# Performance work log

Measured on AMD Instinct MI355X. Metric: run time of the kernel, lower is better.

Reference implementation:

```python
import jax, jax.numpy as jnp
import numpy as np

D = 512        # feat_dim
H_ENC = 8      # motion_encoder heads
H_SA = 4       # semantic-aware attention heads
BS, L, N = 8, 512, 4096
LN_EPS = 1e-5


def _layernorm(x, g, b):
    m = jnp.mean(x, axis=-1, keepdims=True)
    v = jnp.var(x, axis=-1, keepdims=True)
    return (x - m) * jax.lax.rsqrt(v + LN_EPS) * g + b


def _linear(x, w, b):
    # torch nn.Linear convention: w [out, in]
    return x @ w.T + b


def setup_inputs() -> dict:
    key = jax.random.key(0)
    ks = jax.random.split(key, 24)
    s = 0.02
    inp = {
        "motion": jax.random.normal(ks[0], (BS, L, D), jnp.float32),
        "scene_xyz": jax.random.normal(ks[1], (BS, N, 3), jnp.float32),
        "scene_feats": jax.random.normal(ks[2], (BS, N, D), jnp.float32),
        "spatial_prior": jax.random.normal(ks[3], (BS, L, N), jnp.float32),
        # motion_encoder (pre-norm MHA + pre-norm MLP, both residual)
        "enc_ln1_g": jnp.ones((D,), jnp.float32),
        "enc_ln1_b": jnp.zeros((D,), jnp.float32),
        "enc_qkv_w": jax.random.normal(ks[4], (3 * D, D), jnp.float32) * s,
        "enc_qkv_b": jnp.zeros((3 * D,), jnp.float32),
        "enc_out_w": jax.random.normal(ks[5], (D, D), jnp.float32) * s,
        "enc_out_b": jnp.zeros((D,), jnp.float32),
        "enc_ln2_g": jnp.ones((D,), jnp.float32),
        "enc_ln2_b": jnp.zeros((D,), jnp.float32),
        "enc_ff1_w": jax.random.normal(ks[6], (D, D), jnp.float32) * s,
        "enc_ff1_b": jnp.zeros((D,), jnp.float32),
        "enc_ff2_w": jax.random.normal(ks[7], (D, D), jnp.float32) * s,
        "enc_ff2_b": jnp.zeros((D,), jnp.float32),
        # SemanticAwareAttention
        "sa_q_w": jax.random.normal(ks[8], (D, D), jnp.float32) * s,
        "sa_q_b": jnp.zeros((D,), jnp.float32),
        "sa_kv_w": jax.random.normal(ks[9], (2 * D, D), jnp.float32) * s,
        "sa_kv_b": jnp.zeros((2 * D,), jnp.float32),
        "sa_out_w": jax.random.normal(ks[10], (D, D), jnp.float32) * s,
        "sa_out_b": jnp.zeros((D,), jnp.float32),
        # final concat-MLP: in 2D -> 4D -> D  (Mlp(2D, D, expansion=4))
        "mlp_fc1_w": jax.random.normal(ks[11], (4 * D, 2 * D), jnp.float32) * s,
        "mlp_fc1_b": jnp.zeros((4 * D,), jnp.float32),
        "mlp_fc2_w": jax.random.normal(ks[12], (D, 4 * D), jnp.float32) * s,
        "mlp_fc2_b": jnp.zeros((D,), jnp.float32),
    }
    return inp


def _forward(motion, scene_xyz, scene_feats, spatial_prior,
             enc_ln1_g, enc_ln1_b, enc_qkv_w, enc_qkv_b, enc_out_w, enc_out_b,
             enc_ln2_g, enc_ln2_b, enc_ff1_w, enc_ff1_b, enc_ff2_w, enc_ff2_b,
             sa_q_w, sa_q_b, sa_kv_w, sa_kv_b, sa_out_w, sa_out_b,
             mlp_fc1_w, mlp_fc1_b, mlp_fc2_w, mlp_fc2_b):
    bs, slen, _ = motion.shape
    n = scene_feats.shape[1]
    dh_enc = D // H_ENC
    dh_sa = D // H_SA

    # ---- motion encoder: pre-norm MHA + residual ----
    h = _layernorm(motion, enc_ln1_g, enc_ln1_b)
    qkv = _linear(h, enc_qkv_w, enc_qkv_b)                      # [bs, L, 3D]
    q, k, v = jnp.split(qkv, 3, axis=-1)
    q = q.reshape(bs, slen, H_ENC, dh_enc)
    k = k.reshape(bs, slen, H_ENC, dh_enc)
    v = v.reshape(bs, slen, H_ENC, dh_enc)
    att = jnp.einsum("bqhd,bkhd->bhqk", q, k) * (dh_enc ** -0.5)
    att = jax.nn.softmax(att, axis=-1)
    o = jnp.einsum("bhqk,bkhd->bqhd", att, v).reshape(bs, slen, D)
    x = motion + _linear(o, enc_out_w, enc_out_b)

    # ---- pre-norm MLP + residual ----
    h2 = _layernorm(x, enc_ln2_g, enc_ln2_b)
    ff = _linear(jax.nn.gelu(_linear(h2, enc_ff1_w, enc_ff1_b), approximate=False),
                 enc_ff2_w, enc_ff2_b)
    motion_sca = x + ff

    # ---- SemanticAwareAttention ----
    q = _linear(motion_sca, sa_q_w, sa_q_b) * (D ** -0.5)       # scale by feat_dim (faithful)
    kv = _linear(scene_feats, sa_kv_w, sa_kv_b)
    k, v = jnp.split(kv, 2, axis=-1)
    # faithful to torch: q.view(bs, H, L, d) splits heads from flattened (L, D)
    q = q.reshape(bs, H_SA, slen, dh_sa)
    k = k.reshape(bs, n, H_SA, dh_sa).transpose(0, 2, 1, 3)     # [bs, H, N, d]
    v = v.reshape(bs, n, H_SA, dh_sa).transpose(0, 2, 1, 3)
    att = jnp.einsum("bhqd,bhkd->bhqk", q, k) + spatial_prior[:, None, :, :]
    att = jax.nn.softmax(att, axis=-1)
    sm = jnp.einsum("bhqk,bhkd->bqhd", att, v).reshape(bs, slen, D)
    sm_feature = _linear(sm, sa_out_w, sa_out_b)

    # ---- concat + MLP ----
    cat = jnp.concatenate([motion_sca, sm_feature], axis=-1)    # [bs, L, 2D]
    out = _linear(jax.nn.gelu(_linear(cat, mlp_fc1_w, mlp_fc1_b), approximate=False),
                  mlp_fc2_w, mlp_fc2_b)
    return out


def reference(motion, scene_xyz, scene_feats, spatial_prior,
              enc_ln1_g, enc_ln1_b, enc_qkv_w, enc_qkv_b, enc_out_w, enc_out_b,
              enc_ln2_g, enc_ln2_b, enc_ff1_w, enc_ff1_b, enc_ff2_w, enc_ff2_b,
              sa_q_w, sa_q_b, sa_kv_w, sa_kv_b, sa_out_w, sa_out_b,
              mlp_fc1_w, mlp_fc1_b, mlp_fc2_w, mlp_fc2_b):
    return _forward(motion, scene_xyz, scene_feats, spatial_prior,
                    enc_ln1_g, enc_ln1_b, enc_qkv_w, enc_qkv_b, enc_out_w, enc_out_b,
                    enc_ln2_g, enc_ln2_b, enc_ff1_w, enc_ff1_b, enc_ff2_w, enc_ff2_b,
                    sa_q_w, sa_q_b, sa_kv_w, sa_kv_b, sa_out_w, sa_out_b,
                    mlp_fc1_w, mlp_fc1_b, mlp_fc2_w, mlp_fc2_b)
```

## Files before the change

kernel.cpp:

```cpp
#include <hip/hip_runtime.h>

typedef unsigned short bf16_t;
typedef __attribute__((ext_vector_type(8))) short bf16x8;
typedef __attribute__((ext_vector_type(4))) float f32x4;

__device__ __forceinline__ float bf2f(bf16_t u) {
  union { unsigned int i; float f; } v; v.i = ((unsigned int)u) << 16; return v.f;
}
__device__ __forceinline__ bf16_t f2bf(float f) {
  union { float f; unsigned int i; } v; v.f = f;
  unsigned int u = v.i;
  u += 0x7fffu + ((u >> 16) & 1u);
  return (bf16_t)(u >> 16);
}
__device__ __forceinline__ float gelu_exact(float x) {
  return 0.5f * x * (1.0f + erff(x * 0.7071067811865475f));
}
__device__ __forceinline__ void g2l16(bf16_t* l, const bf16_t* g) {
  __builtin_amdgcn_global_load_lds(
      (const __attribute__((address_space(1))) unsigned int*)g,
      (__attribute__((address_space(3))) unsigned int*)l, 16, 0, 0);
}

__global__ __launch_bounds__(256) void f2bf_kernel(const float4* __restrict__ s,
                                                   ushort4* __restrict__ d, int n4) {
  int i = blockIdx.x * 256 + threadIdx.x;
  if (i < n4) {
    float4 f = s[i];
    ushort4 u; u.x = f2bf(f.x); u.y = f2bf(f.y); u.z = f2bf(f.z); u.w = f2bf(f.w);
    d[i] = u;
  }
}

__global__ __launch_bounds__(256) void ln_kernel(const float* __restrict__ x,
                                                 const float* __restrict__ g,
                                                 const float* __restrict__ bta,
                                                 bf16_t* __restrict__ y) {
  const int w = threadIdx.x >> 6, lane = threadIdx.x & 63;
  const long row = (long)blockIdx.x * 4 + w;
  const long base = row * 512;
  const int c0 = lane << 2;
  float v[8];
  float4 f0 = *(const float4*)(x + base + c0);
  float4 f1 = *(const float4*)(x + base + 256 + c0);
  v[0]=f0.x; v[1]=f0.y; v[2]=f0.z; v[3]=f0.w;
  v[4]=f1.x; v[5]=f1.y; v[6]=f1.z; v[7]=f1.w;
  float s = 0.f;
#pragma unroll
  for (int c=0;c<8;++c) s += v[c];
#pragma unroll
  for (int o=32;o>0;o>>=1) s += __shfl_xor(s, o);
  const float mean = s * 0.001953125f;
  float ss = 0.f;
#pragma unroll
  for (int c=0;c<8;++c) { float d = v[c]-mean; ss += d*d; }
#pragma unroll
  for (int o=32;o>0;o>>=1) ss += __shfl_xor(ss, o);
  const float rstd = rsqrtf(ss * 0.001953125f + 1e-5f);
  ushort4 o0, o1;
  o0.x = f2bf((v[0]-mean)*rstd*g[c0+0] + bta[c0+0]);
  o0.y = f2bf((v[1]-mean)*rstd*g[c0+1] + bta[c0+1]);
  o0.z = f2bf((v[2]-mean)*rstd*g[c0+2] + bta[c0+2]);
  o0.w = f2bf((v[3]-mean)*rstd*g[c0+3] + bta[c0+3]);
  o1.x = f2bf((v[4]-mean)*rstd*g[256+c0+0] + bta[256+c0+0]);
  o1.y = f2bf((v[5]-mean)*rstd*g[256+c0+1] + bta[256+c0+1]);
  o1.z = f2bf((v[6]-mean)*rstd*g[256+c0+2] + bta[256+c0+2]);
  o1.w = f2bf((v[7]-mean)*rstd*g[256+c0+3] + bta[256+c0+3]);
  *(ushort4*)(y + base + c0) = o0;
  *(ushort4*)(y + base + 256 + c0) = o1;
}

struct MmaNT {
  const bf16_t* A; const bf16_t* W; const float* bias; const float* res; void* C;
  long lda, sAb, sAh;
  long ldw, sWb, sWh;
  long ldr, sRb, sRh;
  long ldc, sCb, sCh;
  int K, zdiv, cBf, act;
  float scale;
};

template <int MT>
__global__ __launch_bounds__(256) void mma_nt_kernel(MmaNT p) {
  constexpr int FM = MT / 32;
  constexpr int TILE_E = (MT + 128) * 32;
  constexpr int ST_E = MT * 128;
  constexpr int SM_E = (TILE_E > ST_E) ? TILE_E : ST_E;
  __shared__ __align__(16) bf16_t smem[SM_E];
  bf16_t* Al = smem;
  bf16_t* Wl = smem + MT * 32;
  const int tid = threadIdx.x;
  const int wid = tid >> 6, lane = tid & 63;
  const int wm = wid & 1, wn = wid >> 1;
  const int quad = lane >> 4, l16 = lane & 15;
  const int z = blockIdx.z;
  const int zb = z / p.zdiv, zh = z % p.zdiv;

  const int nbx = gridDim.x;
  const int nwg = nbx * gridDim.y;
  const int flat = blockIdx.y * nbx + blockIdx.x;
  const int sw = (flat & 7) * (nwg >> 3) + (flat >> 3);
  const int bx = sw % nbx, by = sw / nbx;

  const long m0 = (long)by * MT;
  const long n0 = (long)bx * 128;

  f32x4 zero4 = {0.f, 0.f, 0.f, 0.f};
  f32x4 acc[FM][4];
#pragma unroll
  for (int fm = 0; fm < FM; ++fm)
#pragma unroll
    for (int fn = 0; fn < 4; ++fn) acc[fm][fn] = zero4;

  if constexpr (MT == 128) {
    const bf16_t* Ag = p.A + (long)zb * p.sAb + (long)zh * p.sAh + m0 * p.lda;
    const bf16_t* Wg = p.W + (long)zb * p.sWb + (long)zh * p.sWh + n0 * p.ldw;
    const int sr = lane >> 2;
    const int sc = (lane & 3) * 8;
    for (int kc = 0; kc < p.K; kc += 32) {
#pragma unroll
      for (int j = 0; j < 2; ++j)
        g2l16(&Al[(j * 64 + wid * 16) * 32],
              Ag + (long)(j * 64 + wid * 16 + sr) * p.lda + kc + sc);
#pragma unroll
      for (int j = 0; j < 2; ++j)
        g2l16(&Wl[(j * 64 + wid * 16) * 32],
              Wg + (long)(j * 64 + wid * 16 + sr) * p.ldw + kc + sc);
      __syncthreads();
      bf16x8 af[FM], wf[4];
#pragma unroll
      for (int fm = 0; fm < FM; ++fm)
        af[fm] = *(const bf16x8*)&Al[(wm * 64 + fm * 16 + l16) * 32 + quad * 8];
#pragma unroll
      for (int fn = 0; fn < 4; ++fn)
        wf[fn] = *(const bf16x8*)&Wl[(wn * 64 + fn * 16 + l16) * 32 + quad * 8];
#pragma unroll
      for (int fm = 0; fm < FM; ++fm)
#pragma unroll
        for (int fn = 0; fn < 4; ++fn)
          acc[fm][fn] = __builtin_amdgcn_mfma_f32_16x16x32_bf16(af[fm], wf[fn], acc[fm][fn], 0, 0, 0);
      __syncthreads();
    }
  } else {
    const bf16_t* Ag = p.A + (long)zb * p.sAb + (long)zh * p.sAh +
                       (m0 + wm * (MT / 2) + l16) * p.lda;
    const bf16_t* Wg = p.W + (long)zb * p.sWb + (long)zh * p.sWh +
                       (n0 + wn * 64 + l16) * p.ldw;
    bf16x8 af[FM], wf[4];
#pragma unroll
    for (int fm = 0; fm < FM; ++fm)
      af[fm] = *(const bf16x8*)(Ag + (long)(fm * 16) * p.lda + quad * 8);
#pragma unroll
    for (int fn = 0; fn < 4; ++fn)
      wf[fn] = *(const bf16x8*)(Wg + (long)(fn * 16) * p.ldw + quad * 8);
    for (int kc = 0; kc < p.K; kc += 32) {
      bf16x8 afn[FM], wfn[4];
      const int kn = kc + 32;
      if (kn < p.K) {
#pragma unroll
        for (int fm = 0; fm < FM; ++fm)
          afn[fm] = *(const bf16x8*)(Ag + (long)(fm * 16) * p.lda + kn + quad * 8);
#pragma unroll
        for (int fn = 0; fn < 4; ++fn)
          wfn[fn] = *(const bf16x8*)(Wg + (long)(fn * 16) * p.ldw + kn + quad * 8);
      }
#pragma unroll
      for (int fm = 0; fm < FM; ++fm)
#pragma unroll
        for (int fn = 0; fn < 4; ++fn)
          acc[fm][fn] = __builtin_amdgcn_mfma_f32_16x16x32_bf16(af[fm], wf[fn], acc[fm][fn], 0, 0, 0);
#pragma unroll
      for (int fm = 0; fm < FM; ++fm) af[fm] = afn[fm];
#pragma unroll
      for (int fn = 0; fn < 4; ++fn) wf[fn] = wfn[fn];
    }
  }

  const long cOff = (long)zb * p.sCb + (long)zh * p.sCh;
  const long rOff = (long)zb * p.sRb + (long)zh * p.sRh;
  if (p.cBf) {
#pragma unroll
    for (int fm = 0; fm < FM; ++fm) {
#pragma unroll
      for (int fn = 0; fn < 4; ++fn) {
        const int lc = wn * 64 + fn * 16 + l16;
        const long col = n0 + lc;
        const float bv = p.bias ? p.bias[col] : 0.f;
#pragma unroll
        for (int r = 0; r < 4; ++r) {
          const int lr = wm * (MT / 2) + fm * 16 + quad * 4 + r;
          float t = acc[fm][fn][r] + bv;
          if (p.act) t = gelu_exact(t);
          t *= p.scale;
          if (p.res) t += p.res[rOff + (m0 + lr) * p.ldr + col];
          smem[lr * 128 + lc] = f2bf(t);
        }
      }
    }
    __syncthreads();
    bf16_t* Cg = (bf16_t*)p.C + cOff + m0 * p.ldc + n0;
#pragma unroll
    for (int i = 0; i < MT / 16; ++i) {
      const int flat2 = tid + i * 256;
      const int r = flat2 >> 4, c = (flat2 & 15) * 8;
      *(uint4*)(Cg + (long)r * p.ldc + c) = *(const uint4*)&smem[r * 128 + c];
    }
  } else {
#pragma unroll
    for (int fm = 0; fm < FM; ++fm) {
#pragma unroll
      for (int fn = 0; fn < 4; ++fn) {
        const long col = n0 + wn * 64 + fn * 16 + l16;
        const float bv = p.bias ? p.bias[col] : 0.f;
#pragma unroll
        for (int r = 0; r < 4; ++r) {
          const long row = m0 + wm * (MT / 2) + fm * 16 + quad * 4 + r;
          float t = acc[fm][fn][r] + bv;
          if (p.act) t = gelu_exact(t);
          t *= p.scale;
          if (p.res) t += p.res[rOff + row * p.ldr + col];
          ((float*)p.C)[cOff + row * p.ldc + col] = t;
        }
      }
    }
  }
}

struct TransP {
  const bf16_t* src; bf16_t* dst;
  long sSb, sSh, ld;
  int nh, N, D;
};

__global__ __launch_bounds__(256) void transpose_kernel(TransP p) {
  __shared__ bf16_t T[64][72];
  const int tid = threadIdx.x;
  const int z = blockIdx.z;
  const int zb = z / p.nh, zh = z % p.nh;
  const long n0 = (long)blockIdx.x * 64;
  const long d0 = (long)blockIdx.y * 64;
  const bf16_t* src = p.src + (long)zb * p.sSb + (long)zh * p.sSh;
  bf16_t* dst = p.dst + (long)z * p.D * p.N;
#pragma unroll
  for (int i = 0; i < 2; ++i) {
    int flat = tid + i * 256, r = flat >> 3, cg = flat & 7;
    uint4 v = *(const uint4*)(src + (n0 + r) * p.ld + d0 + cg * 8);
    *(uint4*)&T[r][cg * 8] = v;
  }
  __syncthreads();
#pragma unroll
  for (int i = 0; i < 2; ++i) {
    int flat = tid + i * 256, dr = flat >> 3, ncg = flat & 7;
    uint4 o;
    unsigned int* op = (unsigned int*)&o;
#pragma unroll
    for (int j = 0; j < 4; ++j)
      op[j] = (unsigned int)T[ncg * 8 + 2 * j][dr] | ((unsigned int)T[ncg * 8 + 2 * j + 1][dr] << 16);
    *(uint4*)(dst + (d0 + dr) * p.N + n0 + ncg * 8) = o;
  }
}

struct FlashP2 {
  const bf16_t* Q; const bf16_t* K; const bf16_t* VT; const float* prior;
  float* partO; float* partML;
  long ldq, sQb, sQh;
  long ldk, sKb, sKh;
  long sVz, sPb;
  int nh, N, segN;
  float scale;
};

template <int DH, int HASP>
__global__ __launch_bounds__(256) void flash3_kernel(FlashP2 p) {
  constexpr int KK = DH / 32;
  constexpr int NFO = DH / 16;
  constexpr int KPAD = DH + 8;
  __shared__ bf16_t smem[64 * KPAD + DH * 72];
  bf16_t* Kl = smem;
  bf16_t* Pl = smem;
  bf16_t* Vl = smem + 64 * KPAD;
  const int tid = threadIdx.x;
  const int w = tid >> 6, lane = tid & 63;
  const int quad = lane >> 4, l16 = lane & 15;
  const int z = blockIdx.z;
  const int zb = z / p.nh, zh = z % p.nh;
  const int qr0 = blockIdx.y * 64 + w * 16;
  const bf16_t* Q = p.Q + (long)zb * p.sQb + (long)zh * p.sQh + (long)qr0 * p.ldq;
  const bf16_t* K = p.K + (long)zb * p.sKb + (long)zh * p.sKh;
  const bf16_t* VT = p.VT + (long)z * p.sVz;

  bf16x8 qf[KK];
#pragma unroll
  for (int kk = 0; kk < KK; ++kk)
    qf[kk] = *(const bf16x8*)(Q + (long)l16 * p.ldq + kk * 32 + quad * 8);

  f32x4 zero4 = {0.f, 0.f, 0.f, 0.f};
  f32x4 O[NFO];
  float m_[4], l_[4];
#pragma unroll
  for (int f = 0; f < NFO; ++f) O[f] = zero4;
#pragma unroll
  for (int r = 0; r < 4; ++r) { m_[r] = -1e30f; l_[r] = 0.f; }

  const int k0 = blockIdx.x * p.segN;
  for (int kt = k0; kt < k0 + p.segN; kt += 64) {
    __syncthreads();
    constexpr int KTH = DH / 8;
#pragma unroll
    for (int i = 0; i < DH / 32; ++i) {
      int flat = tid + i * 256, r = flat / KTH, c = (flat % KTH) * 8;
      *(uint4*)&Kl[r * KPAD + c] = *(const uint4*)(K + (long)(kt + r) * p.ldk + c);
    }
#pragma unroll
    for (int i = 0; i < DH / 32; ++i) {
      int flat = tid + i * 256, r = flat >> 3, c = (flat & 7) * 8;
      *(uint4*)&Vl[r * 72 + c] = *(const uint4*)(VT + (long)r * p.N + kt + c);
    }
    float pr[4][4];
    if (HASP) {
      const float* PR = p.prior + (long)zb * p.sPb +
                        (long)(qr0 + quad * 4) * p.N + kt;
#pragma unroll
      for (int nf = 0; nf < 4; ++nf)
#pragma unroll
        for (int r = 0; r < 4; ++r)
          pr[nf][r] = PR[(long)r * p.N + nf * 16 + l16];
    }
    __syncthreads();
    f32x4 s[4];
#pragma unroll
    for (int nf = 0; nf < 4; ++nf) s[nf] = zero4;
#pragma unroll
    for (int nf = 0; nf < 4; ++nf)
#pragma unroll
      for (int kk = 0; kk < KK; ++kk) {
        bf16x8 kf = *(const bf16x8*)&Kl[(nf * 16 + l16) * KPAD + kk * 32 + quad * 8];
        s[nf] = __builtin_amdgcn_mfma_f32_16x16x32_bf16(qf[kk], kf, s[nf], 0, 0, 0);
      }
    float tm[4];
#pragma unroll
    for (int r = 0; r < 4; ++r) tm[r] = -1e30f;
#pragma unroll
    for (int nf = 0; nf < 4; ++nf)
#pragma unroll
      for (int r = 0; r < 4; ++r) {
        float t = s[nf][r] * p.scale;
        if (HASP) t += pr[nf][r];
        s[nf][r] = t;
        tm[r] = fmaxf(tm[r], t);
      }
#pragma unroll
    for (int off = 1; off < 16; off <<= 1)
#pragma unroll
      for (int r = 0; r < 4; ++r) tm[r] = fmaxf(tm[r], __shfl_xor(tm[r], off));
    float alpha[4], rs[4];
#pragma unroll
    for (int r = 0; r < 4; ++r) {
      float mn = fmaxf(m_[r], tm[r]);
      alpha[r] = __expf(m_[r] - mn);
      m_[r] = mn;
      rs[r] = 0.f;
    }
#pragma unroll
    for (int nf = 0; nf < 4; ++nf)
#pragma unroll
      for (int r = 0; r < 4; ++r) {
        float pv = __expf(s[nf][r] - m_[r]);
        s[nf][r] = pv;
        rs[r] += pv;
      }
#pragma unroll
    for (int off = 1; off < 16; off <<= 1)
#pragma unroll
      for (int r = 0; r < 4; ++r) rs[r] += __shfl_xor(rs[r], off);
#pragma unroll
    for (int r = 0; r < 4; ++r) l_[r] = l_[r] * alpha[r] + rs[r];
    __syncthreads();
#pragma unroll
    for (int nf = 0; nf < 4; ++nf)
#pragma unroll
      for (int r = 0; r < 4; ++r)
        Pl[(w * 16 + quad * 4 + r) * 72 + nf * 16 + l16] = f2bf(s[nf][r]);
#pragma unroll
    for (int f = 0; f < NFO; ++f)
#pragma unroll
      for (int r = 0; r < 4; ++r) O[f][r] *= alpha[r];
    bf16x8 pf[2];
#pragma unroll
    for (int kk2 = 0; kk2 < 2; ++kk2)
      pf[kk2] = *(const bf16x8*)&Pl[(w * 16 + l16) * 72 + kk2 * 32 + quad * 8];
#pragma unroll
    for (int f = 0; f < NFO; ++f)
#pragma unroll
      for (int kk2 = 0; kk2 < 2; ++kk2) {
        bf16x8 vf = *(const bf16x8*)&Vl[(f * 16 + l16) * 72 + kk2 * 32 + quad * 8];
        O[f] = __builtin_amdgcn_mfma_f32_16x16x32_bf16(pf[kk2], vf, O[f], 0, 0, 0);
      }
  }
  const long t = ((long)z * gridDim.y + blockIdx.y) * gridDim.x + blockIdx.x;
  float* PO = p.partO + t * (64 * DH);
  float* PM = p.partML + t * 128;
  const int row = w * 16 + quad * 4;
#pragma unroll
  for (int f = 0; f < NFO; ++f)
#pragma unroll
    for (int r = 0; r < 4; ++r)
      PO[(long)(row + r) * DH + f * 16 + l16] = O[f][r];
  if (l16 == 0) {
#pragma unroll
    for (int r = 0; r < 4; ++r) {
      PM[(row + r) * 2 + 0] = m_[r];
      PM[(row + r) * 2 + 1] = l_[r];
    }
  }
}

struct MergeP {
  const float* partO; const float* partML; bf16_t* C;
  long ldc, sCb;
  int nh, y;
};

template <int DH, int NS>
__global__ __launch_bounds__(256) void fmerge_kernel(MergeP p) {
  const int tid = threadIdx.x;
  const int r = tid >> 2, ch = tid & 3;
  const int blk = blockIdx.x;
  const int z = blk / p.y, qb = blk % p.y;
  const int zb = z / p.nh, zh = z % p.nh;
  const long t0 = (long)blk * NS;
  float mm[NS], wgt[NS];
  float mstar = -1e30f;
#pragma unroll
  for (int s = 0; s < NS; ++s) {
    mm[s] = p.partML[(t0 + s) * 128 + r * 2];
    mstar = fmaxf(mstar, mm[s]);
  }
  float lsum = 0.f;
#pragma unroll
  for (int s = 0; s < NS; ++s) {
    wgt[s] = __expf(mm[s] - mstar);
    lsum += wgt[s] * p.partML[(t0 + s) * 128 + r * 2 + 1];
  }
  const float inv = 1.0f / lsum;
  const int c0 = ch * (DH / 4);
  bf16_t* Cp = p.C + (long)zb * p.sCb + (long)(qb * 64 + r) * p.ldc + (long)zh * DH + c0;
#pragma unroll
  for (int c = 0; c < DH / 4; c += 4) {
    float4 acc = make_float4(0.f, 0.f, 0.f, 0.f);
#pragma unroll
    for (int s = 0; s < NS; ++s) {
      float4 v = *(const float4*)(p.partO + (t0 + s) * (64 * DH) + (long)r * DH + c0 + c);
      acc.x += wgt[s] * v.x; acc.y += wgt[s] * v.y;
      acc.z += wgt[s] * v.z; acc.w += wgt[s] * v.w;
    }
    ushort4 o;
    o.x = f2bf(acc.x * inv); o.y = f2bf(acc.y * inv);
    o.z = f2bf(acc.z * inv); o.w = f2bf(acc.w * inv);
    *(ushort4*)(Cp + c) = o;
  }
}

#define MB(x) ((long)(x) << 20)

extern "C" void kernel_launch(void* const* d_in, const int* in_sizes, int n_in,
                              void* d_out, int out_size, void* d_ws, size_t ws_size,
                              hipStream_t stream) {
  const float* motion      = (const float*)d_in[0];
  const float* scene_feats = (const float*)d_in[2];
  const float* prior       = (const float*)d_in[3];
  const float* ln1_g = (const float*)d_in[4];
  const float* ln1_b = (const float*)d_in[5];
  const float* qkv_w = (const float*)d_in[6];
  const float* qkv_b = (const float*)d_in[7];
  const float* out_w = (const float*)d_in[8];
  const float* out_b = (const float*)d_in[9];
  const float* ln2_g = (const float*)d_in[10];
  const float* ln2_b = (const float*)d_in[11];
  const float* ff1_w = (const float*)d_in[12];
  const float* ff1_b = (const float*)d_in[13];
  const float* ff2_w = (const float*)d_in[14];
  const float* ff2_b = (const float*)d_in[15];
  const float* saq_w = (const float*)d_in[16];
  const float* saq_b = (const float*)d_in[17];
  const float* sakv_w = (const float*)d_in[18];
  const float* sakv_b = (const float*)d_in[19];
  const float* saout_w = (const float*)d_in[20];
  const float* saout_b = (const float*)d_in[21];
  const float* fc1_w = (const float*)d_in[22];
  const float* fc1_b = (const float*)d_in[23];
  const float* fc2_w = (const float*)d_in[24];
  const float* fc2_b = (const float*)d_in[25];

  char* W = (char*)d_ws;
  bf16_t* h_bf    = (bf16_t*)(W + MB(0));
  float*  x_f     = (float*) (W + MB(4));
  bf16_t* o_ff    = (bf16_t*)(W + MB(12));
  bf16_t* qkv_bf  = (bf16_t*)(W + MB(16));
  bf16_t* qsa     = (bf16_t*)(W + MB(28));
  bf16_t* sm_bf   = (bf16_t*)(W + MB(32));
  bf16_t* cat_bf  = (bf16_t*)(W + MB(36));
  bf16_t* fc1g    = (bf16_t*)(W + MB(44));
  bf16_t* vTe     = (bf16_t*)(W + MB(60));
  bf16_t* kv_bf   = (bf16_t*)(W + MB(64));
  bf16_t* vT      = (bf16_t*)(W + MB(128));
  bf16_t* wbase   = (bf16_t*)(W + MB(160));
  bf16_t* scene_bf= (bf16_t*)(W + MB(172));

  float* encO  = (float*)fc1g;
  float* encML = (float*)cat_bf;
  float* saO   = (float*)scene_bf;
  float* saML  = (float*)vTe;

  bf16_t* wq   = wbase + 0L;
  bf16_t* wout = wbase + 786432L;
  bf16_t* wff1 = wbase + 1048576L;
  bf16_t* wff2 = wbase + 1310720L;
  bf16_t* wsaq = wbase + 1572864L;
  bf16_t* wskv = wbase + 1835008L;
  bf16_t* wsout= wbase + 2359296L;
  bf16_t* wfc1 = wbase + 2621440L;
  bf16_t* wfc2 = wbase + 4718592L;

  const dim3 B256(256);
  auto cvt = [&](const float* s, bf16_t* d, long n) {
    int n4 = (int)(n / 4);
    f2bf_kernel<<<(n4 + 255) / 256, B256, 0, stream>>>((const float4*)s, (ushort4*)d, n4);
  };
  cvt(qkv_w,  wq,   786432);
  cvt(out_w,  wout, 262144);
  cvt(ff1_w,  wff1, 262144);
  cvt(ff2_w,  wff2, 262144);
  cvt(saq_w,  wsaq, 262144);
  cvt(sakv_w, wskv, 524288);
  cvt(saout_w,wsout,262144);
  cvt(fc1_w,  wfc1, 2097152);
  cvt(fc2_w,  wfc2, 1048576);
  cvt(scene_feats, scene_bf, 16777216);

  ln_kernel<<<1024, B256, 0, stream>>>(motion, ln1_g, ln1_b, h_bf);

  { MmaNT p{}; p.scale=1.f; p.zdiv=1; p.cBf=1;
    p.A=h_bf; p.lda=512; p.W=wq; p.ldw=512; p.bias=qkv_b;
    p.C=qkv_bf; p.ldc=1536; p.K=512;
    mma_nt_kernel<128><<<dim3(12,32,1), B256, 0, stream>>>(p); }

  { TransP t{}; t.src=qkv_bf+1024; t.dst=vTe; t.sSb=786432; t.sSh=64;
    t.ld=1536; t.nh=8; t.N=512; t.D=64;
    transpose_kernel<<<dim3(8,1,64), B256, 0, stream>>>(t); }
  { FlashP2 p{};
    p.Q=qkv_bf;     p.ldq=1536; p.sQb=786432; p.sQh=64;
    p.K=qkv_bf+512; p.ldk=1536; p.sKb=786432; p.sKh=64;
    p.VT=vTe; p.sVz=32768;
    p.prior=nullptr; p.sPb=0;
    p.partO=encO; p.partML=encML;
    p.nh=8; p.N=512; p.segN=256; p.scale=0.125f;
    flash3_kernel<64,0><<<dim3(2,8,64), B256, 0, stream>>>(p); }
  { MergeP m{}; m.partO=encO; m.partML=encML; m.C=o_ff;
    m.ldc=512; m.sCb=262144; m.nh=8; m.y=8;
    fmerge_kernel<64,2><<<512, B256, 0, stream>>>(m); }

  { MmaNT p{}; p.scale=1.f; p.zdiv=1;
    p.A=o_ff; p.lda=512; p.W=wout; p.ldw=512; p.bias=out_b;
    p.res=motion; p.ldr=512;
    p.C=x_f; p.ldc=512; p.K=512;
    mma_nt_kernel<64><<<dim3(4,64,1), B256, 0, stream>>>(p); }

  ln_kernel<<<1024, B256, 0, stream>>>(x_f, ln2_g, ln2_b, h_bf);

  { MmaNT p{}; p.scale=1.f; p.zdiv=1; p.cBf=1; p.act=1;
    p.A=h_bf; p.lda=512; p.W=wff1; p.ldw=512; p.bias=ff1_b;
    p.C=o_ff; p.ldc=512; p.K=512;
    mma_nt_kernel<64><<<dim3(4,64,1), B256, 0, stream>>>(p); }

  { MmaNT p{}; p.scale=1.f; p.zdiv=1; p.cBf=1;
    p.A=o_ff; p.lda=512; p.W=wff2; p.ldw=512; p.bias=ff2_b;
    p.res=x_f; p.ldr=512;
    p.C=cat_bf; p.ldc=1024; p.K=512;
    mma_nt_kernel<64><<<dim3(4,64,1), B256, 0, stream>>>(p); }

  { MmaNT p{}; p.zdiv=1; p.cBf=1; p.scale=0.04419417382415922f;
    p.A=cat_bf; p.lda=1024; p.W=wsaq; p.ldw=512; p.bias=saq_b;
    p.C=qsa; p.ldc=512; p.K=512;
    mma_nt_kernel<64><<<dim3(4,64,1), B256, 0, stream>>>(p); }

  { MmaNT p{}; p.scale=1.f; p.zdiv=1; p.cBf=1;
    p.A=scene_bf; p.lda=512; p.W=wskv; p.ldw=512; p.bias=sakv_b;
    p.C=kv_bf; p.ldc=1024; p.K=512;
    mma_nt_kernel<128><<<dim3(8,256,1), B256, 0, stream>>>(p); }

  { TransP t{}; t.src=kv_bf+512; t.dst=vT; t.sSb=4194304; t.sSh=128;
    t.ld=1024; t.nh=4; t.N=4096; t.D=128;
    transpose_kernel<<<dim3(64,2,32), B256, 0, stream>>>(t); }
  { FlashP2 p{};
    p.Q=qsa;   p.ldq=128;  p.sQb=262144;  p.sQh=65536;
    p.K=kv_bf; p.ldk=1024; p.sKb=4194304; p.sKh=128;
    p.VT=vT; p.sVz=524288;
    p.prior=prior; p.sPb=2097152;
    p.partO=saO; p.partML=saML;
    p.nh=4; p.N=4096; p.segN=1024; p.scale=1.f;
    flash3_kernel<128,1><<<dim3(4,8,32), B256, 0, stream>>>(p); }
  { MergeP m{}; m.partO=saO; m.partML=saML; m.C=sm_bf;
    m.ldc=512; m.sCb=262144; m.nh=4; m.y=8;
    fmerge_kernel<128,4><<<256, B256, 0, stream>>>(m); }

  { MmaNT p{}; p.scale=1.f; p.zdiv=1; p.cBf=1;
    p.A=sm_bf; p.lda=512; p.W=wsout; p.ldw=512; p.bias=saout_b;
    p.C=cat_bf + 512; p.ldc=1024; p.K=512;
    mma_nt_kernel<64><<<dim3(4,64,1), B256, 0, stream>>>(p); }

  { MmaNT p{}; p.scale=1.f; p.zdiv=1; p.cBf=1; p.act=1;
    p.A=cat_bf; p.lda=1024; p.W=wfc1; p.ldw=1024; p.bias=fc1_b;
    p.C=fc1g; p.ldc=2048; p.K=1024;
    mma_nt_kernel<128><<<dim3(16,32,1), B256, 0, stream>>>(p); }

  { MmaNT p{}; p.scale=1.f; p.zdiv=1;
    p.A=fc1g; p.lda=2048; p.W=wfc2; p.ldw=2048; p.bias=fc2_b;
    p.C=d_out; p.ldc=512; p.K=2048;
    mma_nt_kernel<64><<<dim3(4,64,1), B256, 0, stream>>>(p); }
}
```

Measured before the change: 700.0 us.

## Register-prefetch next K/V/prior tile during flash attention compute

Restructures the flash attention key loop as a software pipeline. The next K tile, transposed V tile and spatial-prior values are loaded into registers while the current tile's QK and PV MFMAs run. They are written to shared memory only after a barrier at the end of the iteration. This hides global-load latency behind compute, at the cost of extra VGPRs for the staging buffers, which may reduce occupancy, especially for large head dimensions.

```diff
diff --git a/kernel.cpp b/kernel.cpp
--- a/kernel.cpp
+++ b/kernel.cpp
@@ -275,6 +275,8 @@
   constexpr int KK = DH / 32;
   constexpr int NFO = DH / 16;
   constexpr int KPAD = DH + 8;
+  constexpr int NST = DH / 32;
+  constexpr int KTH = DH / 8;
   __shared__ bf16_t smem[64 * KPAD + DH * 72];
   bf16_t* Kl = smem;
   bf16_t* Pl = smem;
@@ -303,30 +305,64 @@
   for (int r = 0; r < 4; ++r) { m_[r] = -1e30f; l_[r] = 0.f; }
 
   const int k0 = blockIdx.x * p.segN;
-  for (int kt = k0; kt < k0 + p.segN; kt += 64) {
-    __syncthreads();
-    constexpr int KTH = DH / 8;
-#pragma unroll
-    for (int i = 0; i < DH / 32; ++i) {
-      int flat = tid + i * 256, r = flat / KTH, c = (flat % KTH) * 8;
-      *(uint4*)&Kl[r * KPAD + c] = *(const uint4*)(K + (long)(kt + r) * p.ldk + c);
-    }
-#pragma unroll
-    for (int i = 0; i < DH / 32; ++i) {
-      int flat = tid + i * 256, r = flat >> 3, c = (flat & 7) * 8;
-      *(uint4*)&Vl[r * 72 + c] = *(const uint4*)(VT + (long)r * p.N + kt + c);
-    }
-    float pr[4][4];
-    if (HASP) {
-      const float* PR = p.prior + (long)zb * p.sPb +
-                        (long)(qr0 + quad * 4) * p.N + kt;
-#pragma unroll
-      for (int nf = 0; nf < 4; ++nf)
-#pragma unroll
-        for (int r = 0; r < 4; ++r)
-          pr[nf][r] = PR[(long)r * p.N + nf * 16 + l16];
-    }
-    __syncthreads();
+  const int kend = k0 + p.segN;
+
+  uint4 kst[NST], vst[NST];
+  float pr[4][4], prN[4][4];
+
+#pragma unroll
+  for (int i = 0; i < NST; ++i) {
+    int fl = tid + i * 256, r = fl / KTH, c = (fl % KTH) * 8;
+    kst[i] = *(const uint4*)(K + (long)(k0 + r) * p.ldk + c);
+  }
+#pragma unroll
+  for (int i = 0; i < NST; ++i) {
+    int fl = tid + i * 256, r = fl >> 3, c = (fl & 7) * 8;
+    vst[i] = *(const uint4*)(VT + (long)r * p.N + k0 + c);
+  }
+  if (HASP) {
+    const float* PR = p.prior + (long)zb * p.sPb + (long)(qr0 + quad * 4) * p.N + k0;
+#pragma unroll
+    for (int nf = 0; nf < 4; ++nf)
+#pragma unroll
+      for (int r = 0; r < 4; ++r)
+        pr[nf][r] = PR[(long)r * p.N + nf * 16 + l16];
+  }
+#pragma unroll
+  for (int i = 0; i < NST; ++i) {
+    int fl = tid + i * 256, r = fl / KTH, c = (fl % KTH) * 8;
+    *(uint4*)&Kl[r * KPAD + c] = kst[i];
+  }
+#pragma unroll
+  for (int i = 0; i < NST; ++i) {
+    int fl = tid + i * 256, r = fl >> 3, c = (fl & 7) * 8;
+    *(uint4*)&Vl[r * 72 + c] = vst[i];
+  }
+  __syncthreads();
+
+  for (int kt = k0; kt < kend; kt += 64) {
+    const int kn = kt + 64;
+    const bool haveNext = (kn < kend);
+    if (haveNext) {
+#pragma unroll
+      for (int i = 0; i < NST; ++i) {
+        int fl = tid + i * 256, r = fl / KTH, c = (fl % KTH) * 8;
+        kst[i] = *(const uint4*)(K + (long)(kn + r) * p.ldk + c);
+      }
+#pragma unroll
+      for (int i = 0; i < NST; ++i) {
+        int fl = tid + i * 256, r = fl >> 3, c = (fl & 7) * 8;
+        vst[i] = *(const uint4*)(VT + (long)r * p.N + kn + c);
+      }
+      if (HASP) {
+        const float* PR = p.prior + (long)zb * p.sPb + (long)(qr0 + quad * 4) * p.N + kn;
+#pragma unroll
+        for (int nf = 0; nf < 4; ++nf)
+#pragma unroll
+          for (int r = 0; r < 4; ++r)
+            prN[nf][r] = PR[(long)r * p.N + nf * 16 + l16];
+      }
+    }
     f32x4 s[4];
 #pragma unroll
     for (int nf = 0; nf < 4; ++nf) s[nf] = zero4;
@@ -396,6 +432,27 @@
         bf16x8 vf = *(const bf16x8*)&Vl[(f * 16 + l16) * 72 + kk2 * 32 + quad * 8];
         O[f] = __builtin_amdgcn_mfma_f32_16x16x32_bf16(pf[kk2], vf, O[f], 0, 0, 0);
       }
+    __syncthreads();
+    if (haveNext) {
+#pragma unroll
+      for (int i = 0; i < NST; ++i) {
+        int fl = tid + i * 256, r = fl / KTH, c = (fl % KTH) * 8;
+        *(uint4*)&Kl[r * KPAD + c] = kst[i];
+      }
+#pragma unroll
+      for (int i = 0; i < NST; ++i) {
+        int fl = tid + i * 256, r = fl >> 3, c = (fl & 7) * 8;
+        *(uint4*)&Vl[r * 72 + c] = vst[i];
+      }
+      if (HASP) {
+#pragma unroll
+        for (int nf = 0; nf < 4; ++nf)
+#pragma unroll
+          for (int r = 0; r < 4; ++r)
+            pr[nf][r] = prN[nf][r];
+      }
+      __syncthreads();
+    }
   }
   const long t = ((long)z * gridDim.y + blockIdx.y) * gridDim.x + blockIdx.x;
   float* PO = p.partO + t * (64 * DH);
```

After: 861.9 us. 23.1% more time.

## Load flash K/V tiles via direct global-to-LDS with XOR swizzle

Applied to the files above, without the earlier changes.

Replaces the register-staged K and V^T tile copies in the flash attention kernel with global_load_lds direct-to-LDS transfers. Row padding is replaced by an XOR swizzle on column offsets to avoid bank conflicts. For head dims other than 128, P gets its own LDS region so the barrier before writing P can be dropped. This removes VGPR round-trips and one sync per tile, at the cost of more LDS for smaller heads and tighter coupling between the swizzle and the lane mapping.

```diff
diff --git a/kernel.cpp b/kernel.cpp
--- a/kernel.cpp
+++ b/kernel.cpp
@@ -274,11 +274,14 @@
 __global__ __launch_bounds__(256) void flash3_kernel(FlashP2 p) {
   constexpr int KK = DH / 32;
   constexpr int NFO = DH / 16;
-  constexpr int KPAD = DH + 8;
-  __shared__ bf16_t smem[64 * KPAD + DH * 72];
+  constexpr int KE = 64 * DH;
+  constexpr int VE = DH * 64;
+  constexpr int PE = 64 * 72;
+  constexpr int SM_E = (DH == 128) ? (KE + VE) : (KE + VE + PE);
+  __shared__ __align__(16) bf16_t smem[SM_E];
   bf16_t* Kl = smem;
-  bf16_t* Pl = smem;
-  bf16_t* Vl = smem + 64 * KPAD;
+  bf16_t* Vl = smem + KE;
+  bf16_t* Pl = (DH == 128) ? smem : (smem + KE + VE);
   const int tid = threadIdx.x;
   const int w = tid >> 6, lane = tid & 63;
   const int quad = lane >> 4, l16 = lane & 15;
@@ -302,19 +305,29 @@
 #pragma unroll
   for (int r = 0; r < 4; ++r) { m_[r] = -1e30f; l_[r] = 0.f; }
 
+  constexpr int LPR = DH / 8;
+  constexpr int RPC = 512 / DH;
+  const int krl = lane / LPR;
+  const int kcb = (lane % LPR) * 16;
+  const int vrl = lane >> 3;
+  const int vcb = (lane & 7) * 16;
+
   const int k0 = blockIdx.x * p.segN;
   for (int kt = k0; kt < k0 + p.segN; kt += 64) {
     __syncthreads();
-    constexpr int KTH = DH / 8;
-#pragma unroll
-    for (int i = 0; i < DH / 32; ++i) {
-      int flat = tid + i * 256, r = flat / KTH, c = (flat % KTH) * 8;
-      *(uint4*)&Kl[r * KPAD + c] = *(const uint4*)(K + (long)(kt + r) * p.ldk + c);
-    }
-#pragma unroll
-    for (int i = 0; i < DH / 32; ++i) {
-      int flat = tid + i * 256, r = flat >> 3, c = (flat & 7) * 8;
-      *(uint4*)&Vl[r * 72 + c] = *(const uint4*)(VT + (long)r * p.N + kt + c);
+#pragma unroll
+    for (int j = 0; j < DH / 32; ++j) {
+      const int R0 = (w + 4 * j) * RPC;
+      const int r = R0 + krl;
+      const int cs = kcb ^ ((r & 7) << 4);
+      g2l16(&Kl[R0 * DH], K + (long)(kt + r) * p.ldk + (cs >> 1));
+    }
+#pragma unroll
+    for (int j = 0; j < DH / 32; ++j) {
+      const int R0 = (w + 4 * j) * 8;
+      const int r = R0 + vrl;
+      const int cs = vcb ^ ((r & 7) << 4);
+      g2l16(&Vl[R0 * 64], VT + (long)r * p.N + kt + (cs >> 1));
     }
     float pr[4][4];
     if (HASP) {
@@ -334,7 +347,8 @@
     for (int nf = 0; nf < 4; ++nf)
 #pragma unroll
       for (int kk = 0; kk < KK; ++kk) {
-        bf16x8 kf = *(const bf16x8*)&Kl[(nf * 16 + l16) * KPAD + kk * 32 + quad * 8];
+        bf16x8 kf = *(const bf16x8*)&Kl[(nf * 16 + l16) * DH +
+                                        ((kk * 32 + quad * 8) ^ ((l16 & 7) << 3))];
         s[nf] = __builtin_amdgcn_mfma_f32_16x16x32_bf16(qf[kk], kf, s[nf], 0, 0, 0);
       }
     float tm[4];
@@ -375,7 +389,7 @@
       for (int r = 0; r < 4; ++r) rs[r] += __shfl_xor(rs[r], off);
 #pragma unroll
     for (int r = 0; r < 4; ++r) l_[r] = l_[r] * alpha[r] + rs[r];
-    __syncthreads();
+    if (DH == 128) __syncthreads();
 #pragma unroll
     for (int nf = 0; nf < 4; ++nf)
 #pragma unroll
@@ -393,7 +407,8 @@
     for (int f = 0; f < NFO; ++f)
 #pragma unroll
       for (int kk2 = 0; kk2 < 2; ++kk2) {
-        bf16x8 vf = *(const bf16x8*)&Vl[(f * 16 + l16) * 72 + kk2 * 32 + quad * 8];
+        bf16x8 vf = *(const bf16x8*)&Vl[(f * 16 + l16) * 64 +
+                                        ((kk2 * 32 + quad * 8) ^ ((l16 & 7) << 3))];
         O[f] = __builtin_amdgcn_mfma_f32_16x16x32_bf16(pf[kk2], vf, O[f], 0, 0, 0);
       }
   }
```

Measured after the change: 684.4 us. -2.2%, faster.
